# Kernel tuning notes

Hardware: AMD Instinct MI355X
Metric: run time of the kernel (lower is better)

Reference implementation:

```python
import jax, jax.numpy as jnp
import numpy as np

B, L, D_MODEL = 4, 4096, 1024
D_STATE, D_CONV, N_HEADS, CHUNK = 16, 4, 8, 64
D_INNER = 2048
HEADDIM = D_INNER // N_HEADS
CONV_DIM = D_INNER + 2 * D_STATE
D_PROJ = 2 * D_INNER + 2 * D_STATE + N_HEADS
EPS = 1e-5


def _silu(v):
    return v * jax.nn.sigmoid(v)


def _segsum(x):
    # x: (..., T) -> (..., T, T); segsum[i,j] = sum_{j<d<=i} x[d], -inf above diag
    T = x.shape[-1]
    xe = jnp.broadcast_to(x[..., None], (*x.shape, T))
    lower_strict = jnp.tril(jnp.ones((T, T), bool), -1)
    s = jnp.cumsum(jnp.where(lower_strict, xe, 0.0), axis=-2)
    lower = jnp.tril(jnp.ones((T, T), bool), 0)
    return jnp.where(lower, s, -jnp.inf)


def _ssd(x, A, Bm, Cm, chunk):
    # x: (b,l,h,p), A: (b,l,h), Bm/Cm: (b,l,n) (single B/C shared across heads)
    b, l, h, p = x.shape
    n = Bm.shape[-1]
    c = l // chunk
    x = x.reshape(b, c, chunk, h, p)
    A = A.reshape(b, c, chunk, h).transpose(0, 3, 1, 2)  # b h c l
    Bc = Bm.reshape(b, c, chunk, n)
    Cc = Cm.reshape(b, c, chunk, n)
    A_cs = jnp.cumsum(A, axis=-1)                        # b h c l
    Lmat = jnp.exp(_segsum(A))                           # b h c l s
    Y_diag = jnp.einsum('bcln,bcsn,bhcls,bcshp->bclhp', Cc, Bc, Lmat, x)
    decay_states = jnp.exp(A_cs[..., -1:] - A_cs)        # b h c l
    states = jnp.einsum('bcln,bhcl,bclhp->bchpn', Bc, decay_states, x)
    states = jnp.concatenate([jnp.zeros_like(states[:, :1]), states], axis=1)
    A_last = jnp.pad(A_cs[..., -1], ((0, 0), (0, 0), (1, 0)))  # b h (c+1)
    decay_chunk = jnp.exp(_segsum(A_last))               # b h (c+1) (c+1)
    new_states = jnp.einsum('bhzc,bchpn->bzhpn', decay_chunk, states)
    states_prev, final_state = new_states[:, :-1], new_states[:, -1]
    Y_off = jnp.einsum('bcln,bchpn,bhcl->bclhp', Cc, states_prev, jnp.exp(A_cs))
    Y = (Y_diag + Y_off).reshape(b, l, h, p)
    return Y, final_state


def setup_inputs() -> dict:
    key = jax.random.key(0)
    ks = jax.random.split(key, 8)
    inp = {
        'input_tensor': jax.random.normal(ks[0], (B, L, D_MODEL), dtype=jnp.float32),
        'W_in': jax.random.normal(ks[1], (D_PROJ, D_MODEL), dtype=jnp.float32) / np.sqrt(D_MODEL),
        'conv_w': jax.random.normal(ks[2], (CONV_DIM, 1, D_CONV), dtype=jnp.float32) * 0.2,
        'conv_b': jax.random.normal(ks[3], (CONV_DIM,), dtype=jnp.float32) * 0.02,
        'dt_bias': jax.random.uniform(ks[4], (N_HEADS,), dtype=jnp.float32) * 0.1,
        'log_A': jnp.log(jnp.arange(1, N_HEADS + 1, dtype=jnp.float32)),
        'D_skip': jnp.ones((N_HEADS,), dtype=jnp.float32),
        'norm_w': jnp.ones((D_INNER,), dtype=jnp.float32),
        'W_out': jax.random.normal(ks[5], (D_MODEL, D_INNER), dtype=jnp.float32) / np.sqrt(D_INNER),
    }
    return inp


def reference(input_tensor, W_in, conv_w, conv_b, dt_bias, log_A, D_skip, norm_w, W_out):
    bsz, slen, _ = input_tensor.shape
    proj = input_tensor @ W_in.T  # (b,l,D_PROJ)
    z = proj[..., :D_INNER]
    xBC = proj[..., D_INNER:D_INNER + CONV_DIM]
    dt = jax.nn.softplus(proj[..., D_INNER + CONV_DIM:] + dt_bias)  # (b,l,h)
    # causal depthwise conv1d (torch pads both sides then slices [:, :slen])
    xt = jnp.transpose(xBC, (0, 2, 1))  # (b,d,l)
    conv = jax.lax.conv_general_dilated(
        xt, conv_w, window_strides=(1,), padding=[(D_CONV - 1, 0)],
        feature_group_count=CONV_DIM) + conv_b[None, :, None]
    xBC = _silu(jnp.transpose(conv, (0, 2, 1)))
    x = xBC[..., :D_INNER]
    Bm = xBC[..., D_INNER:D_INNER + D_STATE]
    Cm = xBC[..., D_INNER + D_STATE:]
    A = jnp.broadcast_to((-jnp.exp(log_A))[None, None, :], (bsz, slen, N_HEADS))
    xh = x.reshape(bsz, slen, N_HEADS, HEADDIM) * dt[..., None]
    Y, _ = _ssd(xh, A, Bm, Cm, CHUNK)
    Y = Y + xh * D_skip[:, None]
    y = Y.reshape(bsz, slen, D_INNER)
    # gated RMSNorm
    y = y * _silu(z)
    y = y * jax.lax.rsqrt(jnp.mean(y * y, axis=-1, keepdims=True) + EPS) * norm_w
    return y @ W_out.T
```

## Files before the change

### kernel.cpp

```cpp
#include <hip/hip_runtime.h>
#include <hip/hip_bf16.h>
#include <math.h>

#define BATCH   4
#define SEQLEN  4096
#define DMODEL  1024
#define DSTATE  16
#define DCONV   4
#define NHEADS  8
#define CHUNKSZ 64
#define DINNER  2048
#define HEADDIM 256
#define CONVDIM 2080
#define DPROJ   4136
#define NPADW   4352
#define LDP     4224
#define ROWS    (BATCH*SEQLEN)
#define NCHUNK  (SEQLEN/CHUNKSZ)

typedef unsigned short bf16_t;
typedef __attribute__((ext_vector_type(8))) short bfrag;
typedef __attribute__((ext_vector_type(4))) float f32x4;

__device__ __forceinline__ float sigmoidf_(float v) { return 1.0f / (1.0f + __expf(-v)); }
__device__ __forceinline__ float siluf_(float v)    { return v * sigmoidf_(v); }
__device__ __forceinline__ float softplusf_(float v) {
    return fmaxf(v, 0.f) + log1pf(__expf(-fabsf(v)));
}

__device__ __forceinline__ float bf2f(bf16_t u) {
    union { unsigned int i; float f; } v; v.i = ((unsigned int)u) << 16; return v.f;
}
__device__ __forceinline__ float bflo(unsigned int u) {
    union { unsigned int i; float f; } v; v.i = u << 16; return v.f;
}
__device__ __forceinline__ float bfhi(unsigned int u) {
    union { unsigned int i; float f; } v; v.i = u & 0xffff0000u; return v.f;
}
__device__ __forceinline__ bf16_t f2bf(float f) {
    unsigned int x = __float_as_uint(f);
    unsigned int r = (x + 0x7fffu + ((x >> 16) & 1u)) >> 16;
    return (bf16_t)r;
}
__device__ __forceinline__ unsigned int pack2(float a, float b) {
    return (unsigned int)f2bf(a) | ((unsigned int)f2bf(b) << 16);
}

__device__ __forceinline__ void async_copy16(const bf16_t* g, bf16_t* l) {
    __builtin_amdgcn_global_load_lds(
        (const __attribute__((address_space(1))) void*)g,
        (__attribute__((address_space(3))) void*)l, 16, 0, 0);
}

template<int N>
__device__ __forceinline__ void wait_vmcnt() {
    __builtin_amdgcn_s_waitcnt(0x0F70 | N);
}
__device__ __forceinline__ void barrier_() {
    __builtin_amdgcn_s_barrier();
    asm volatile("" ::: "memory");
}

__global__ __launch_bounds__(256)
void cvt_f32_bf16(const float* __restrict__ src, bf16_t* __restrict__ dst, int n8)
{
    int i = blockIdx.x * 256 + threadIdx.x;
    if (i >= n8) return;
    float4 a = *(const float4*)&src[(size_t)i * 8];
    float4 b = *(const float4*)&src[(size_t)i * 8 + 4];
    uint4 o;
    o.x = pack2(a.x, a.y); o.y = pack2(a.z, a.w);
    o.z = pack2(b.x, b.y); o.w = pack2(b.z, b.w);
    *(uint4*)&dst[(size_t)i * 8] = o;
}

__global__ __launch_bounds__(256)
void cvt_pad_w1(const float* __restrict__ src, bf16_t* __restrict__ dst)
{
    int i = blockIdx.x * 256 + threadIdx.x;
    if (i >= NPADW * DMODEL / 4) return;
    size_t e = (size_t)i * 4;
    int row = (int)(e >> 10);
    ushort4 o = make_ushort4(0, 0, 0, 0);
    if (row < DPROJ) {
        float4 v = *(const float4*)&src[e];
        o.x = f2bf(v.x); o.y = f2bf(v.y); o.z = f2bf(v.z); o.w = f2bf(v.w);
    }
    *(ushort4*)&dst[e] = o;
}

__global__ __launch_bounds__(256)
void cvt_w2(const float* __restrict__ W, const float* __restrict__ norm_w,
            bf16_t* __restrict__ dst)
{
    int i = blockIdx.x * 256 + threadIdx.x;
    if (i >= DMODEL * DINNER / 4) return;
    size_t e = (size_t)i * 4;
    int k = (int)(e & (DINNER - 1));
    float4 v = *(const float4*)&W[e];
    float4 w = *(const float4*)&norm_w[k];
    ushort4 o;
    o.x = f2bf(v.x * w.x); o.y = f2bf(v.y * w.y);
    o.z = f2bf(v.z * w.z); o.w = f2bf(v.w * w.w);
    *(ushort4*)&dst[e] = o;
}

__device__ __forceinline__
void ld_afrags(bfrag (&af)[4][2], const bf16_t* base, int wmqi, int fr, int quad)
{
    #pragma unroll
    for (int i2 = 0; i2 < 4; ++i2)
        #pragma unroll
        for (int kk = 0; kk < 2; ++kk)
            af[i2][kk] = *(const bfrag*)
                &base[(wmqi + i2*16 + fr)*64 + (((kk*4 + quad) ^ (fr & 7)) * 8)];
}
__device__ __forceinline__
void ld_bfrags(bfrag (&bf_)[2][2], const bf16_t* base, int wnqj, int fr, int quad)
{
    #pragma unroll
    for (int j2 = 0; j2 < 2; ++j2)
        #pragma unroll
        for (int kk = 0; kk < 2; ++kk)
            bf_[j2][kk] = *(const bfrag*)
                &base[(wnqj + j2*16 + fr)*64 + (((kk*4 + quad) ^ (fr & 7)) * 8)];
}
template<int QI, int QJ>
__device__ __forceinline__
void mm8(f32x4 (&acc)[8][4], const bfrag (&af)[4][2], const bfrag (&bf_)[2][2])
{
    __builtin_amdgcn_s_setprio(1);
    #pragma unroll
    for (int i2 = 0; i2 < 4; ++i2)
        #pragma unroll
        for (int j2 = 0; j2 < 2; ++j2)
            #pragma unroll
            for (int kk = 0; kk < 2; ++kk)
                acc[QI*4 + i2][QJ*2 + j2] = __builtin_amdgcn_mfma_f32_16x16x32_bf16(
                    af[i2][kk], bf_[j2][kk], acc[QI*4 + i2][QJ*2 + j2], 0, 0, 0);
    __builtin_amdgcn_s_setprio(0);
}

template<bool OUT_BF16>
__device__ __forceinline__
void gemm256_body(const bf16_t* __restrict__ A, const bf16_t* __restrict__ W,
                  void* __restrict__ Cv, const float* __restrict__ rowScale,
                  int Nstore, int K, int lda, int ldw, int ldc)
{
    __shared__ __align__(16) bf16_t smem[65536];
    bf16_t* As = smem;
    bf16_t* Ws = smem + 32768;

    const int tid  = threadIdx.x;
    const int wave = tid >> 6, lane = tid & 63;
    const int quad = lane >> 4, fr = lane & 15;
    const int ln3  = lane >> 3;
    const int cswz = ((lane & 7) ^ ln3) * 8;

    const int gx   = gridDim.x;
    const int nwg  = gx * gridDim.y;
    const int flat = blockIdx.y * gx + blockIdx.x;
    const int q8   = nwg >> 3;
    const int swz  = (flat & 7) * q8 + (flat >> 3);
    const int col0 = (swz % gx) * 256;
    const int row0 = (swz / gx) * 256;

    const int wm = (wave >> 2) * 128, wn = (wave & 3) * 64;

    const bf16_t* gA[2][2];
    const bf16_t* gW[2][2];
    #pragma unroll
    for (int h = 0; h < 2; ++h)
        #pragma unroll
        for (int q = 0; q < 2; ++q) {
            int rA = 128*q + 8*wave + 64*h;
            int rB = 128*q + 64*(wave >> 2) + 8*(wave & 3) + 32*h;
            gA[h][q] = A + (size_t)(row0 + rA + ln3) * lda + cswz;
            gW[h][q] = W + (size_t)(col0 + rB + ln3) * ldw + cswz;
        }

#define STG_A(H, Q, NB, K0S)                                                     \
    async_copy16(gA[H][Q] + (K0S),                                               \
                 &As[(NB)*16384 + (128*(Q) + 8*wave + 64*(H))*64])
#define STG_B(H, Q, NB, K0S)                                                     \
    async_copy16(gW[H][Q] + (K0S),                                               \
                 &Ws[(NB)*16384 + (128*(Q) + 64*(wave>>2) + 8*(wave&3) + 32*(H))*64])

    f32x4 acc[8][4];
    #pragma unroll
    for (int i = 0; i < 8; ++i)
        #pragma unroll
        for (int j = 0; j < 4; ++j) {
            f32x4 z = {0.f, 0.f, 0.f, 0.f};
            acc[i][j] = z;
        }
    bfrag af[4][2], bf_[2][2];

    STG_A(0,0,0,0); STG_A(0,1,0,0);
    STG_B(0,0,0,0); STG_B(0,1,0,0);
    STG_B(1,0,0,0); STG_B(1,1,0,0);
    STG_A(1,0,0,0); STG_A(1,1,0,0);

#define TILE_STEP(BUF_, NB_, K0S_, STG_, V1_, V2_) do {                          \
          \
    wait_vmcnt<4>(); barrier_();                                                 \
    ld_afrags(af, &As[(BUF_)*16384], wm, fr, quad);                              \
    ld_bfrags(bf_, &Ws[(BUF_)*16384], wn, fr, quad);                             \
    if (STG_) { STG_A(0,0,NB_,K0S_); STG_A(0,1,NB_,K0S_); }                      \
    mm8<0,0>(acc, af, bf_);                                                      \
                                                     \
    wait_vmcnt<V1_>(); barrier_();                                               \
    ld_bfrags(bf_, &Ws[(BUF_)*16384], wn + 32, fr, quad);                        \
    if (STG_) { STG_B(0,0,NB_,K0S_); STG_B(0,1,NB_,K0S_); }                      \
    mm8<0,1>(acc, af, bf_);                                                      \
                                                     \
    wait_vmcnt<V2_>(); barrier_();                                               \
    ld_afrags(af, &As[(BUF_)*16384], wm + 64, fr, quad);                         \
    if (STG_) { STG_B(1,0,NB_,K0S_); STG_B(1,1,NB_,K0S_); }                      \
    mm8<1,1>(acc, af, bf_);                                                      \
                                     \
    barrier_();                                                                  \
    ld_bfrags(bf_, &Ws[(BUF_)*16384], wn, fr, quad);                             \
    if (STG_) { STG_A(1,0,NB_,K0S_); STG_A(1,1,NB_,K0S_); }                      \
    mm8<1,0>(acc, af, bf_);                                                      \
} while (0)

    const int nt = K >> 6;
    for (int t = 0; t < nt - 1; ++t) {
        TILE_STEP((t & 1), ((t & 1) ^ 1), ((t + 1) * 64), true, 4, 4);
    }
    TILE_STEP(((nt - 1) & 1), 0, 0, false, 2, 0);

#undef TILE_STEP
#undef STG_A
#undef STG_B

    if (OUT_BF16) {
        __syncthreads();
        bf16_t* C = (bf16_t*)Cv;
        #pragma unroll
        for (int pass = 0; pass < 2; ++pass) {
            if ((wave >> 2) == pass) {
                #pragma unroll
                for (int i = 0; i < 8; ++i)
                    #pragma unroll
                    for (int j = 0; j < 4; ++j) {
                        int col = wn + 16 * j + fr;
                        #pragma unroll
                        for (int r = 0; r < 4; ++r) {
                            int rl = 16 * i + quad * 4 + r;
                            smem[rl * 264 + col] = f2bf(acc[i][j][r]);
                        }
                    }
            }
            __syncthreads();
            #pragma unroll
            for (int k = 0; k < 8; ++k) {
                int id = k * 512 + tid;
                int rl = id >> 5, ch = id & 31;
                if (col0 + ch * 8 < Nstore) {
                    uint4 v = *(const uint4*)&smem[rl * 264 + ch * 8];
                    *(uint4*)&C[(size_t)(row0 + pass * 128 + rl) * ldc
                                + col0 + ch * 8] = v;
                }
            }
            if (pass == 0) __syncthreads();
        }
    } else {
        float rs[8][4];
        #pragma unroll
        for (int i = 0; i < 8; ++i) {
            size_t m = (size_t)row0 + wm + i * 16 + quad * 4;
            #pragma unroll
            for (int r = 0; r < 4; ++r) rs[i][r] = rowScale ? rowScale[m + r] : 1.f;
        }
        float* C = (float*)Cv;
        #pragma unroll
        for (int j = 0; j < 4; ++j) {
            int n = col0 + wn + j * 16 + fr;
            if (n < Nstore) {
                #pragma unroll
                for (int i = 0; i < 8; ++i) {
                    size_t m = (size_t)row0 + wm + i * 16 + quad * 4;
                    #pragma unroll
                    for (int r = 0; r < 4; ++r)
                        C[(m + r) * ldc + n] = acc[i][j][r] * rs[i][r];
                }
            }
        }
    }
}

__global__ __launch_bounds__(512, 2)
void gemm_g1(const bf16_t* __restrict__ A, const bf16_t* __restrict__ W,
             void* __restrict__ Cv, const float* __restrict__ rowScale,
             int Nstore, int K, int lda, int ldw, int ldc)
{ gemm256_body<true>(A, W, Cv, rowScale, Nstore, K, lda, ldw, ldc); }

__global__ __launch_bounds__(512, 2)
void gemm_g2(const bf16_t* __restrict__ A, const bf16_t* __restrict__ W,
             void* __restrict__ Cv, const float* __restrict__ rowScale,
             int Nstore, int K, int lda, int ldw, int ldc)
{ gemm256_body<false>(A, W, Cv, rowScale, Nstore, K, lda, ldw, ldc); }

__global__ __launch_bounds__(256)
void ssd_fused(const bf16_t* __restrict__ proj, const float* __restrict__ conv_w,
               const float* __restrict__ conv_b, const float* __restrict__ dt_bias,
               const float* __restrict__ log_A, const float* __restrict__ D_skip,
               bf16_t* __restrict__ ybuf)
{
    __shared__ float Bc[64][16];
    __shared__ float Cc[64][16];
    __shared__ float Bp[64][16];
    __shared__ float dtc[64];
    __shared__ float dtp[64];
    __shared__ __align__(16) bf16_t sc_b[64][72];
    __shared__ __align__(16) bf16_t xT[256][72];
    __shared__ __align__(16) bf16_t SpT[256][32];
    __shared__ __align__(16) bf16_t A2[64][32];

    const int c = blockIdx.x, h = blockIdx.y, b = blockIdx.z;
    const int t = threadIdx.x;
    const int row0 = b * SEQLEN + c * CHUNKSZ;
    const float a   = -__expf(log_A[h]);
    const float Dsk = D_skip[h];
    const float bias = dt_bias[h];

    {
        int s = t >> 2, ch8 = (t & 3) * 8;
        int l = c * CHUNKSZ + s;
        const bf16_t* base = &proj[(size_t)(row0 + s) * LDP + 4096 + ch8];
        uint4 zz = make_uint4(0, 0, 0, 0);
        uint4 u3 = *(const uint4*)&base[0];
        uint4 u2 = (l >= 1) ? *(const uint4*)&base[-LDP]     : zz;
        uint4 u1 = (l >= 2) ? *(const uint4*)&base[-2 * LDP] : zz;
        uint4 u0 = (l >= 3) ? *(const uint4*)&base[-3 * LDP] : zz;
        float t3[8] = {bflo(u3.x), bfhi(u3.x), bflo(u3.y), bfhi(u3.y),
                       bflo(u3.z), bfhi(u3.z), bflo(u3.w), bfhi(u3.w)};
        float t2[8] = {bflo(u2.x), bfhi(u2.x), bflo(u2.y), bfhi(u2.y),
                       bflo(u2.z), bfhi(u2.z), bflo(u2.w), bfhi(u2.w)};
        float t1[8] = {bflo(u1.x), bfhi(u1.x), bflo(u1.y), bfhi(u1.y),
                       bflo(u1.z), bfhi(u1.z), bflo(u1.w), bfhi(u1.w)};
        float t0[8] = {bflo(u0.x), bfhi(u0.x), bflo(u0.y), bfhi(u0.y),
                       bflo(u0.z), bfhi(u0.z), bflo(u0.w), bfhi(u0.w)};
        #pragma unroll
        for (int j = 0; j < 8; ++j) {
            int ch = ch8 + j;
            float4 w = *(const float4*)&conv_w[(2048 + ch) * 4];
            float av = conv_b[2048 + ch];
            av = fmaf(w.x, t0[j], av);
            av = fmaf(w.y, t1[j], av);
            av = fmaf(w.z, t2[j], av);
            av = fmaf(w.w, t3[j], av);
            float v = siluf_(av);
            if (ch < 16) Bc[s][ch] = v; else Cc[s][ch - 16] = v;
        }
    }
    if (t < 128) {
        int s = t >> 1, ch8 = (t & 1) * 8;
        float vout[8];
        #pragma unroll
        for (int j = 0; j < 8; ++j) vout[j] = 0.f;
        if (c > 0) {
            int l = (c - 1) * CHUNKSZ + s;
            const bf16_t* base = &proj[(size_t)(row0 - CHUNKSZ + s) * LDP + 4096 + ch8];
            uint4 zz = make_uint4(0, 0, 0, 0);
            uint4 u3 = *(const uint4*)&base[0];
            uint4 u2 = (l >= 1) ? *(const uint4*)&base[-LDP]     : zz;
            uint4 u1 = (l >= 2) ? *(const uint4*)&base[-2 * LDP] : zz;
            uint4 u0 = (l >= 3) ? *(const uint4*)&base[-3 * LDP] : zz;
            float t3[8] = {bflo(u3.x), bfhi(u3.x), bflo(u3.y), bfhi(u3.y),
                           bflo(u3.z), bfhi(u3.z), bflo(u3.w), bfhi(u3.w)};
            float t2[8] = {bflo(u2.x), bfhi(u2.x), bflo(u2.y), bfhi(u2.y),
                           bflo(u2.z), bfhi(u2.z), bflo(u2.w), bfhi(u2.w)};
            float t1[8] = {bflo(u1.x), bfhi(u1.x), bflo(u1.y), bfhi(u1.y),
                           bflo(u1.z), bfhi(u1.z), bflo(u1.w), bfhi(u1.w)};
            float t0[8] = {bflo(u0.x), bfhi(u0.x), bflo(u0.y), bfhi(u0.y),
                           bflo(u0.z), bfhi(u0.z), bflo(u0.w), bfhi(u0.w)};
            #pragma unroll
            for (int j = 0; j < 8; ++j) {
                int ch = ch8 + j;
                float4 w = *(const float4*)&conv_w[(2048 + ch) * 4];
                float av = conv_b[2048 + ch];
                av = fmaf(w.x, t0[j], av);
                av = fmaf(w.y, t1[j], av);
                av = fmaf(w.z, t2[j], av);
                av = fmaf(w.w, t3[j], av);
                vout[j] = siluf_(av);
            }
        }
        #pragma unroll
        for (int j = 0; j < 8; ++j) Bp[s][ch8 + j] = vout[j];
    } else if (t < 192) {
        int s = t - 128;
        float v = bf2f(proj[(size_t)(row0 + s) * LDP + 4128 + h]) + bias;
        dtc[s] = softplusf_(v);
    } else {
        int s = t - 192;
        float w = 0.f;
        if (c > 0) {
            float v = bf2f(proj[(size_t)(row0 - CHUNKSZ + s) * LDP + 4128 + h]) + bias;
            w = softplusf_(v) * __expf(a * (float)(63 - s));
        }
        dtp[s] = w;
    }
    __syncthreads();

    {
        int l = t >> 2;
        int sbase = (t & 3) * 16;
        unsigned int pk[8];
        #pragma unroll
        for (int jj = 0; jj < 16; jj += 2) {
            float v0 = 0.f, v1 = 0.f;
            int s0 = sbase + jj, s1 = s0 + 1;
            if (s0 <= l) {
                float dot = 0.f;
                #pragma unroll
                for (int n = 0; n < 16; ++n) dot = fmaf(Cc[l][n], Bc[s0][n], dot);
                v0 = dot * __expf(a * (float)(l - s0));
                if (s0 == l) v0 += Dsk;
            }
            if (s1 <= l) {
                float dot = 0.f;
                #pragma unroll
                for (int n = 0; n < 16; ++n) dot = fmaf(Cc[l][n], Bc[s1][n], dot);
                v1 = dot * __expf(a * (float)(l - s1));
                if (s1 == l) v1 += Dsk;
            }
            pk[jj >> 1] = pack2(v0, v1);
        }
        uint4 u0 = {pk[0], pk[1], pk[2], pk[3]};
        uint4 u1 = {pk[4], pk[5], pk[6], pk[7]};
        *(uint4*)&sc_b[l][sbase]     = u0;
        *(uint4*)&sc_b[l][sbase + 8] = u1;
    }
    if (t < 64) {
        float e = __expf(a * (float)(t + 1));
        unsigned int pk[8];
        #pragma unroll
        for (int n = 0; n < 16; n += 2) pk[n >> 1] = pack2(e * Cc[t][n], e * Cc[t][n + 1]);
        uint4 u0 = {pk[0], pk[1], pk[2], pk[3]};
        uint4 u1 = {pk[4], pk[5], pk[6], pk[7]};
        uint4 zz = make_uint4(0, 0, 0, 0);
        *(uint4*)&A2[t][0]  = u0;
        *(uint4*)&A2[t][8]  = u1;
        *(uint4*)&A2[t][16] = zz;
        *(uint4*)&A2[t][24] = zz;
    }

    {
        const int p = t;
        const int xch = h * HEADDIM + p;
        const float4 w = *(const float4*)&conv_w[(size_t)xch * 4];
        const float cb = conv_b[xch];
        const int colp = 2048 + xch;
        {
            const bf16_t* pr = &proj[(size_t)row0 * LDP + colp];
            int l0 = c * CHUNKSZ;
            float xm3 = (l0 >= 3) ? bf2f(pr[-3 * LDP]) : 0.f;
            float xm2 = (l0 >= 2) ? bf2f(pr[-2 * LDP]) : 0.f;
            float xm1 = (l0 >= 1) ? bf2f(pr[-LDP])     : 0.f;
            #pragma unroll
            for (int s0 = 0; s0 < 64; s0 += 8) {
                float xd[8];
                #pragma unroll
                for (int q = 0; q < 8; ++q) {
                    float xc = bf2f(pr[(size_t)(s0 + q) * LDP]);
                    float av = cb;
                    av = fmaf(w.x, xm3, av);
                    av = fmaf(w.y, xm2, av);
                    av = fmaf(w.z, xm1, av);
                    av = fmaf(w.w, xc, av);
                    xd[q] = siluf_(av) * dtc[s0 + q];
                    xm3 = xm2; xm2 = xm1; xm1 = xc;
                }
                uint4 u;
                u.x = pack2(xd[0], xd[1]); u.y = pack2(xd[2], xd[3]);
                u.z = pack2(xd[4], xd[5]); u.w = pack2(xd[6], xd[7]);
                *(uint4*)&xT[p][s0] = u;
            }
        }
        float Sp[16];
        #pragma unroll
        for (int n = 0; n < 16; ++n) Sp[n] = 0.f;
        if (c > 0) {
            const bf16_t* pr = &proj[(size_t)(row0 - CHUNKSZ) * LDP + colp];
            int l0 = (c - 1) * CHUNKSZ;
            float xm3 = (l0 >= 3) ? bf2f(pr[-3 * LDP]) : 0.f;
            float xm2 = (l0 >= 2) ? bf2f(pr[-2 * LDP]) : 0.f;
            float xm1 = (l0 >= 1) ? bf2f(pr[-LDP])     : 0.f;
            for (int s = 0; s < 64; ++s) {
                float xc = bf2f(pr[(size_t)s * LDP]);
                float av = cb;
                av = fmaf(w.x, xm3, av);
                av = fmaf(w.y, xm2, av);
                av = fmaf(w.z, xm1, av);
                av = fmaf(w.w, xc, av);
                float v = siluf_(av) * dtp[s];
                #pragma unroll
                for (int n = 0; n < 16; ++n) Sp[n] = fmaf(Bp[s][n], v, Sp[n]);
                xm3 = xm2; xm2 = xm1; xm1 = xc;
            }
        }
        unsigned int pk[8];
        #pragma unroll
        for (int n = 0; n < 16; n += 2) pk[n >> 1] = pack2(Sp[n], Sp[n + 1]);
        uint4 u0 = {pk[0], pk[1], pk[2], pk[3]};
        uint4 u1 = {pk[4], pk[5], pk[6], pk[7]};
        uint4 zz = make_uint4(0, 0, 0, 0);
        *(uint4*)&SpT[p][0]  = u0;
        *(uint4*)&SpT[p][8]  = u1;
        *(uint4*)&SpT[p][16] = zz;
        *(uint4*)&SpT[p][24] = zz;
    }
    __syncthreads();

    {
        const int wave = t >> 6, lane = t & 63;
        const int quad = lane >> 4, fr = lane & 15;
        f32x4 acc[4][4];
        #pragma unroll
        for (int i = 0; i < 4; ++i)
            #pragma unroll
            for (int j = 0; j < 4; ++j) {
                f32x4 z = {0.f, 0.f, 0.f, 0.f};
                acc[i][j] = z;
            }
        #pragma unroll
        for (int kk = 0; kk < 2; ++kk) {
            bfrag af[4], bfr[4];
            #pragma unroll
            for (int i = 0; i < 4; ++i)
                af[i] = *(const bfrag*)&sc_b[16 * i + fr][32 * kk + quad * 8];
            #pragma unroll
            for (int j = 0; j < 4; ++j)
                bfr[j] = *(const bfrag*)&xT[64 * wave + 16 * j + fr][32 * kk + quad * 8];
            #pragma unroll
            for (int i = 0; i < 4; ++i)
                #pragma unroll
                for (int j = 0; j < 4; ++j)
                    acc[i][j] = __builtin_amdgcn_mfma_f32_16x16x32_bf16(
                                    af[i], bfr[j], acc[i][j], 0, 0, 0);
        }
        {
            bfrag af[4], bfr[4];
            #pragma unroll
            for (int i = 0; i < 4; ++i)
                af[i] = *(const bfrag*)&A2[16 * i + fr][quad * 8];
            #pragma unroll
            for (int j = 0; j < 4; ++j)
                bfr[j] = *(const bfrag*)&SpT[64 * wave + 16 * j + fr][quad * 8];
            #pragma unroll
            for (int i = 0; i < 4; ++i)
                #pragma unroll
                for (int j = 0; j < 4; ++j)
                    acc[i][j] = __builtin_amdgcn_mfma_f32_16x16x32_bf16(
                                    af[i], bfr[j], acc[i][j], 0, 0, 0);
        }
        __syncthreads();
        bf16_t* buf = &xT[0][0];
        #pragma unroll
        for (int i = 0; i < 4; ++i)
            #pragma unroll
            for (int j = 0; j < 4; ++j) {
                int pc = 64 * wave + 16 * j + fr;
                #pragma unroll
                for (int r = 0; r < 4; ++r) {
                    int l = 16 * i + quad * 4 + r;
                    buf[l * 264 + pc] = f2bf(acc[i][j][r]);
                }
            }
        __syncthreads();
        bf16_t* ybase = &ybuf[(size_t)row0 * DINNER + h * HEADDIM];
        #pragma unroll
        for (int k = 0; k < 8; ++k) {
            int id = k * 256 + t;
            int l = id >> 5, ch = id & 31;
            uint4 v = *(const uint4*)&buf[l * 264 + ch * 8];
            *(uint4*)&ybase[(size_t)l * DINNER + ch * 8] = v;
        }
    }
}

__global__ __launch_bounds__(256)
void gate_kernel(const bf16_t* __restrict__ proj, bf16_t* __restrict__ ybuf,
                 float* __restrict__ rowscale)
{
    __shared__ float red[4];
    int i = blockIdx.x;
    int t = threadIdx.x;
    const bf16_t* zrow = &proj[(size_t)i * LDP];
    bf16_t* yrow = &ybuf[(size_t)i * DINNER];
    uint4 yv = *(const uint4*)&yrow[t * 8];
    uint4 zv = *(const uint4*)&zrow[t * 8];
    float ya[8] = {bflo(yv.x), bfhi(yv.x), bflo(yv.y), bfhi(yv.y),
                   bflo(yv.z), bfhi(yv.z), bflo(yv.w), bfhi(yv.w)};
    float za[8] = {bflo(zv.x), bfhi(zv.x), bflo(zv.y), bfhi(zv.y),
                   bflo(zv.z), bfhi(zv.z), bflo(zv.w), bfhi(zv.w)};
    float g[8];
    float ss = 0.f;
    #pragma unroll
    for (int j = 0; j < 8; ++j) {
        float gv = ya[j] * siluf_(za[j]);
        g[j] = gv;
        ss = fmaf(gv, gv, ss);
    }
    #pragma unroll
    for (int off = 32; off >= 1; off >>= 1) ss += __shfl_down(ss, off);
    if ((t & 63) == 0) red[t >> 6] = ss;
    __syncthreads();
    if (t == 0) {
        float tot = red[0] + red[1] + red[2] + red[3];
        rowscale[i] = rsqrtf(tot / (float)DINNER + 1e-5f);
    }
    uint4 o;
    o.x = pack2(g[0], g[1]); o.y = pack2(g[2], g[3]);
    o.z = pack2(g[4], g[5]); o.w = pack2(g[6], g[7]);
    *(uint4*)&yrow[t * 8] = o;
}

extern "C" void kernel_launch(void* const* d_in, const int* in_sizes, int n_in,
                              void* d_out, int out_size, void* d_ws, size_t ws_size,
                              hipStream_t stream)
{
    const float* input   = (const float*)d_in[0];
    const float* W_in    = (const float*)d_in[1];
    const float* conv_w  = (const float*)d_in[2];
    const float* conv_b  = (const float*)d_in[3];
    const float* dt_bias = (const float*)d_in[4];
    const float* log_A   = (const float*)d_in[5];
    const float* D_skip  = (const float*)d_in[6];
    const float* norm_w  = (const float*)d_in[7];
    const float* W_out   = (const float*)d_in[8];
    float* out = (float*)d_out;

    bf16_t* proj  = (bf16_t*)d_ws;
    bf16_t* region1 = proj + (size_t)ROWS * LDP;
    bf16_t* Wb2   = region1 + (size_t)ROWS * CONVDIM;
    float*  rowscale = (float*)(Wb2 + (size_t)DMODEL * DINNER);
    bf16_t* Ab    = region1;
    bf16_t* Wb1   = Ab + (size_t)ROWS * DMODEL;
    bf16_t* ybuf  = region1;

    size_t need = (size_t)ROWS * LDP * 2 + (size_t)ROWS * CONVDIM * 2
                + (size_t)DMODEL * DINNER * 2 + (size_t)ROWS * 4;
    if (ws_size < need) {
        hipMemsetAsync(d_out, 0, (size_t)out_size * sizeof(float), stream);
        return;
    }

    cvt_f32_bf16<<<(ROWS * DMODEL / 8 + 255) / 256, 256, 0, stream>>>(
        input, Ab, ROWS * DMODEL / 8);
    cvt_pad_w1<<<(NPADW * DMODEL / 4 + 255) / 256, 256, 0, stream>>>(W_in, Wb1);
    cvt_w2<<<(DMODEL * DINNER / 4 + 255) / 256, 256, 0, stream>>>(W_out, norm_w, Wb2);

    dim3 g1(NPADW / 256, ROWS / 256);
    gemm_g1<<<g1, 512, 0, stream>>>(Ab, Wb1, proj, nullptr,
                                    LDP, DMODEL, DMODEL, DMODEL, LDP);
    dim3 gs(NCHUNK, NHEADS, BATCH);
    ssd_fused<<<gs, 256, 0, stream>>>(proj, conv_w, conv_b, dt_bias,
                                      log_A, D_skip, ybuf);
    gate_kernel<<<ROWS, 256, 0, stream>>>(proj, ybuf, rowscale);
    dim3 g2(DMODEL / 256, ROWS / 256);
    gemm_g2<<<g2, 512, 0, stream>>>(ybuf, Wb2, out, rowscale,
                                    DMODEL, DINNER, DINNER, DINNER, DMODEL);
}
```

Measured before the change: 533.3 us.

## Switch GEMMs to 32x32 MFMA and fuse gating/RMS sum into SSD kernel

```diff
diff --git a/kernel.cpp b/kernel.cpp
--- a/kernel.cpp
+++ b/kernel.cpp
@@ -21,6 +21,7 @@
 typedef unsigned short bf16_t;
 typedef __attribute__((ext_vector_type(8))) short bfrag;
 typedef __attribute__((ext_vector_type(4))) float f32x4;
+typedef __attribute__((ext_vector_type(16))) float f32x16;
 
 __device__ __forceinline__ float sigmoidf_(float v) { return 1.0f / (1.0f + __expf(-v)); }
 __device__ __forceinline__ float siluf_(float v)    { return v * sigmoidf_(v); }
@@ -52,10 +53,7 @@
         (__attribute__((address_space(3))) void*)l, 16, 0, 0);
 }
 
-template<int N>
-__device__ __forceinline__ void wait_vmcnt() {
-    __builtin_amdgcn_s_waitcnt(0x0F70 | N);
-}
+#define WAITV(N)  asm volatile("s_waitcnt vmcnt(" #N ")" ::: "memory")
 __device__ __forceinline__ void barrier_() {
     __builtin_amdgcn_s_barrier();
     asm volatile("" ::: "memory");
@@ -106,45 +104,50 @@
 }
 
 __device__ __forceinline__
-void ld_afrags(bfrag (&af)[4][2], const bf16_t* base, int wmqi, int fr, int quad)
-{
+void ld_a32(bfrag (&a)[4][2], const bf16_t* base, int wm, int lane, int k0)
+{
+    const int r5 = lane & 31, hi = lane >> 5;
     #pragma unroll
-    for (int i2 = 0; i2 < 4; ++i2)
-        #pragma unroll
-        for (int kk = 0; kk < 2; ++kk)
-            af[i2][kk] = *(const bfrag*)
-                &base[(wmqi + i2*16 + fr)*64 + (((kk*4 + quad) ^ (fr & 7)) * 8)];
+    for (int ks = 0; ks < 2; ++ks)
+        #pragma unroll
+        for (int rb = 0; rb < 4; ++rb) {
+            int row = wm + rb * 32 + r5;
+            int chunk = (2 * (k0 + ks) + hi) ^ (row & 7);
+            a[rb][ks] = *(const bfrag*)&base[row * 64 + chunk * 8];
+        }
 }
 __device__ __forceinline__
-void ld_bfrags(bfrag (&bf_)[2][2], const bf16_t* base, int wnqj, int fr, int quad)
-{
+void ld_b32(bfrag (&b)[2][2], const bf16_t* base, int wn, int lane, int k0)
+{
+    const int r5 = lane & 31, hi = lane >> 5;
     #pragma unroll
-    for (int j2 = 0; j2 < 2; ++j2)
-        #pragma unroll
-        for (int kk = 0; kk < 2; ++kk)
-            bf_[j2][kk] = *(const bfrag*)
-                &base[(wnqj + j2*16 + fr)*64 + (((kk*4 + quad) ^ (fr & 7)) * 8)];
-}
-template<int QI, int QJ>
+    for (int ks = 0; ks < 2; ++ks)
+        #pragma unroll
+        for (int cb = 0; cb < 2; ++cb) {
+            int row = wn + cb * 32 + r5;
+            int chunk = (2 * (k0 + ks) + hi) ^ (row & 7);
+            b[cb][ks] = *(const bfrag*)&base[row * 64 + chunk * 8];
+        }
+}
 __device__ __forceinline__
-void mm8(f32x4 (&acc)[8][4], const bfrag (&af)[4][2], const bfrag (&bf_)[2][2])
+void mm16(f32x16 (&acc)[4][2], const bfrag (&a)[4][2], const bfrag (&b)[2][2])
 {
     __builtin_amdgcn_s_setprio(1);
     #pragma unroll
-    for (int i2 = 0; i2 < 4; ++i2)
-        #pragma unroll
-        for (int j2 = 0; j2 < 2; ++j2)
-            #pragma unroll
-            for (int kk = 0; kk < 2; ++kk)
-                acc[QI*4 + i2][QJ*2 + j2] = __builtin_amdgcn_mfma_f32_16x16x32_bf16(
-                    af[i2][kk], bf_[j2][kk], acc[QI*4 + i2][QJ*2 + j2], 0, 0, 0);
+    for (int ks = 0; ks < 2; ++ks)
+        #pragma unroll
+        for (int rb = 0; rb < 4; ++rb)
+            #pragma unroll
+            for (int cb = 0; cb < 2; ++cb)
+                acc[rb][cb] = __builtin_amdgcn_mfma_f32_32x32x16_bf16(
+                    a[rb][ks], b[cb][ks], acc[rb][cb], 0, 0, 0);
     __builtin_amdgcn_s_setprio(0);
 }
 
 template<bool OUT_BF16>
 __device__ __forceinline__
 void gemm256_body(const bf16_t* __restrict__ A, const bf16_t* __restrict__ W,
-                  void* __restrict__ Cv, const float* __restrict__ rowScale,
+                  void* __restrict__ Cv, const float* __restrict__ rowSum,
                   int Nstore, int K, int lda, int ldw, int ldc)
 {
     __shared__ __align__(16) bf16_t smem[65536];
@@ -153,7 +156,6 @@
 
     const int tid  = threadIdx.x;
     const int wave = tid >> 6, lane = tid & 63;
-    const int quad = lane >> 4, fr = lane & 15;
     const int ln3  = lane >> 3;
     const int cswz = ((lane & 7) ^ ln3) * 8;
 
@@ -186,55 +188,43 @@
     async_copy16(gW[H][Q] + (K0S),                                               \
                  &Ws[(NB)*16384 + (128*(Q) + 64*(wave>>2) + 8*(wave&3) + 32*(H))*64])
 
-    f32x4 acc[8][4];
+    f32x16 acc[4][2];
     #pragma unroll
-    for (int i = 0; i < 8; ++i)
-        #pragma unroll
-        for (int j = 0; j < 4; ++j) {
-            f32x4 z = {0.f, 0.f, 0.f, 0.f};
-            acc[i][j] = z;
-        }
-    bfrag af[4][2], bf_[2][2];
-
-    STG_A(0,0,0,0); STG_A(0,1,0,0);
-    STG_B(0,0,0,0); STG_B(0,1,0,0);
-    STG_B(1,0,0,0); STG_B(1,1,0,0);
-    STG_A(1,0,0,0); STG_A(1,1,0,0);
-
-#define TILE_STEP(BUF_, NB_, K0S_, STG_, V1_, V2_) do {                          \
-          \
-    wait_vmcnt<4>(); barrier_();                                                 \
-    ld_afrags(af, &As[(BUF_)*16384], wm, fr, quad);                              \
-    ld_bfrags(bf_, &Ws[(BUF_)*16384], wn, fr, quad);                             \
-    if (STG_) { STG_A(0,0,NB_,K0S_); STG_A(0,1,NB_,K0S_); }                      \
-    mm8<0,0>(acc, af, bf_);                                                      \
-                                                     \
-    wait_vmcnt<V1_>(); barrier_();                                               \
-    ld_bfrags(bf_, &Ws[(BUF_)*16384], wn + 32, fr, quad);                        \
-    if (STG_) { STG_B(0,0,NB_,K0S_); STG_B(0,1,NB_,K0S_); }                      \
-    mm8<0,1>(acc, af, bf_);                                                      \
-                                                     \
-    wait_vmcnt<V2_>(); barrier_();                                               \
-    ld_afrags(af, &As[(BUF_)*16384], wm + 64, fr, quad);                         \
-    if (STG_) { STG_B(1,0,NB_,K0S_); STG_B(1,1,NB_,K0S_); }                      \
-    mm8<1,1>(acc, af, bf_);                                                      \
-                                     \
-    barrier_();                                                                  \
-    ld_bfrags(bf_, &Ws[(BUF_)*16384], wn, fr, quad);                             \
-    if (STG_) { STG_A(1,0,NB_,K0S_); STG_A(1,1,NB_,K0S_); }                      \
-    mm8<1,0>(acc, af, bf_);                                                      \
-} while (0)
+    for (int i = 0; i < 4; ++i)
+        #pragma unroll
+        for (int j = 0; j < 2; ++j)
+            #pragma unroll
+            for (int r = 0; r < 16; ++r)
+                acc[i][j][r] = 0.f;
+    bfrag afr[4][2], bfr[2][2];
+
+    STG_A(0,0,0,0); STG_A(0,1,0,0); STG_A(1,0,0,0); STG_A(1,1,0,0);
+    STG_B(0,0,0,0); STG_B(0,1,0,0); STG_B(1,0,0,0); STG_B(1,1,0,0);
 
     const int nt = K >> 6;
-    for (int t = 0; t < nt - 1; ++t) {
-        TILE_STEP((t & 1), ((t & 1) ^ 1), ((t + 1) * 64), true, 4, 4);
-    }
-    TILE_STEP(((nt - 1) & 1), 0, 0, false, 2, 0);
-
-#undef TILE_STEP
+    for (int t = 0; t < nt; ++t) {
+        const int cur = (t & 1) * 16384;
+        const int nb  = (t + 1) & 1;
+        const int ko  = (t + 1) * 64;
+        const bool stg = (t + 1 < nt);
+        WAITV(0);
+        barrier_();
+        ld_a32(afr, As + cur, wm, lane, 0);
+        ld_b32(bfr, Ws + cur, wn, lane, 0);
+        if (stg) { STG_A(0,0,nb,ko); STG_A(0,1,nb,ko);
+                   STG_A(1,0,nb,ko); STG_A(1,1,nb,ko); }
+        mm16(acc, afr, bfr);
+        ld_a32(afr, As + cur, wm, lane, 2);
+        ld_b32(bfr, Ws + cur, wn, lane, 2);
+        if (stg) { STG_B(0,0,nb,ko); STG_B(0,1,nb,ko);
+                   STG_B(1,0,nb,ko); STG_B(1,1,nb,ko); }
+        mm16(acc, afr, bfr);
+    }
+
 #undef STG_A
 #undef STG_B
 
+    const int c32 = lane & 31, hi4 = (lane >> 5) * 4;
     if (OUT_BF16) {
         __syncthreads();
         bf16_t* C = (bf16_t*)Cv;
@@ -242,14 +232,14 @@
         for (int pass = 0; pass < 2; ++pass) {
             if ((wave >> 2) == pass) {
                 #pragma unroll
-                for (int i = 0; i < 8; ++i)
+                for (int rb = 0; rb < 4; ++rb)
                     #pragma unroll
-                    for (int j = 0; j < 4; ++j) {
-                        int col = wn + 16 * j + fr;
+                    for (int cb = 0; cb < 2; ++cb) {
+                        int col = wn + cb * 32 + c32;
                         #pragma unroll
-                        for (int r = 0; r < 4; ++r) {
-                            int rl = 16 * i + quad * 4 + r;
-                            smem[rl * 264 + col] = f2bf(acc[i][j][r]);
+                        for (int reg = 0; reg < 16; ++reg) {
+                            int rl = rb * 32 + (reg & 3) + 8 * (reg >> 2) + hi4;
+                            smem[rl * 264 + col] = f2bf(acc[rb][cb][reg]);
                         }
                     }
             }
@@ -267,24 +257,26 @@
             if (pass == 0) __syncthreads();
         }
     } else {
-        float rs[8][4];
-        #pragma unroll
-        for (int i = 0; i < 8; ++i) {
-            size_t m = (size_t)row0 + wm + i * 16 + quad * 4;
-            #pragma unroll
-            for (int r = 0; r < 4; ++r) rs[i][r] = rowScale ? rowScale[m + r] : 1.f;
-        }
         float* C = (float*)Cv;
         #pragma unroll
-        for (int j = 0; j < 4; ++j) {
-            int n = col0 + wn + j * 16 + fr;
-            if (n < Nstore) {
-                #pragma unroll
-                for (int i = 0; i < 8; ++i) {
-                    size_t m = (size_t)row0 + wm + i * 16 + quad * 4;
+        for (int rb = 0; rb < 4; ++rb) {
+            float rs[16];
+            #pragma unroll
+            for (int reg = 0; reg < 16; ++reg) {
+                size_t m = (size_t)row0 + wm + rb * 32
+                         + (reg & 3) + 8 * (reg >> 2) + hi4;
+                rs[reg] = rowSum ? rsqrtf(rowSum[m] * (1.f / DINNER) + 1e-5f) : 1.f;
+            }
+            #pragma unroll
+            for (int cb = 0; cb < 2; ++cb) {
+                int n = col0 + wn + cb * 32 + c32;
+                if (n < Nstore) {
                     #pragma unroll
-                    for (int r = 0; r < 4; ++r)
-                        C[(m + r) * ldc + n] = acc[i][j][r] * rs[i][r];
+                    for (int reg = 0; reg < 16; ++reg) {
+                        size_t m = (size_t)row0 + wm + rb * 32
+                                 + (reg & 3) + 8 * (reg >> 2) + hi4;
+                        C[m * ldc + n] = acc[rb][cb][reg] * rs[reg];
+                    }
                 }
             }
         }
@@ -293,21 +285,21 @@
 
 __global__ __launch_bounds__(512, 2)
 void gemm_g1(const bf16_t* __restrict__ A, const bf16_t* __restrict__ W,
-             void* __restrict__ Cv, const float* __restrict__ rowScale,
+             void* __restrict__ Cv, const float* __restrict__ rowSum,
              int Nstore, int K, int lda, int ldw, int ldc)
-{ gemm256_body<true>(A, W, Cv, rowScale, Nstore, K, lda, ldw, ldc); }
+{ gemm256_body<true>(A, W, Cv, rowSum, Nstore, K, lda, ldw, ldc); }
 
 __global__ __launch_bounds__(512, 2)
 void gemm_g2(const bf16_t* __restrict__ A, const bf16_t* __restrict__ W,
-             void* __restrict__ Cv, const float* __restrict__ rowScale,
+             void* __restrict__ Cv, const float* __restrict__ rowSum,
              int Nstore, int K, int lda, int ldw, int ldc)
-{ gemm256_body<false>(A, W, Cv, rowScale, Nstore, K, lda, ldw, ldc); }
+{ gemm256_body<false>(A, W, Cv, rowSum, Nstore, K, lda, ldw, ldc); }
 
 __global__ __launch_bounds__(256)
 void ssd_fused(const bf16_t* __restrict__ proj, const float* __restrict__ conv_w,
                const float* __restrict__ conv_b, const float* __restrict__ dt_bias,
                const float* __restrict__ log_A, const float* __restrict__ D_skip,
-               bf16_t* __restrict__ ybuf)
+               bf16_t* __restrict__ ybuf, float* __restrict__ rowsum)
 {
     __shared__ float Bc[64][16];
     __shared__ float Cc[64][16];
@@ -573,51 +565,34 @@
             }
         __syncthreads();
         bf16_t* ybase = &ybuf[(size_t)row0 * DINNER + h * HEADDIM];
+        const bf16_t* zbase = &proj[(size_t)row0 * LDP + h * HEADDIM];
         #pragma unroll
         for (int k = 0; k < 8; ++k) {
             int id = k * 256 + t;
             int l = id >> 5, ch = id & 31;
-            uint4 v = *(const uint4*)&buf[l * 264 + ch * 8];
-            *(uint4*)&ybase[(size_t)l * DINNER + ch * 8] = v;
-        }
-    }
-}
-
-__global__ __launch_bounds__(256)
-void gate_kernel(const bf16_t* __restrict__ proj, bf16_t* __restrict__ ybuf,
-                 float* __restrict__ rowscale)
-{
-    __shared__ float red[4];
-    int i = blockIdx.x;
-    int t = threadIdx.x;
-    const bf16_t* zrow = &proj[(size_t)i * LDP];
-    bf16_t* yrow = &ybuf[(size_t)i * DINNER];
-    uint4 yv = *(const uint4*)&yrow[t * 8];
-    uint4 zv = *(const uint4*)&zrow[t * 8];
-    float ya[8] = {bflo(yv.x), bfhi(yv.x), bflo(yv.y), bfhi(yv.y),
-                   bflo(yv.z), bfhi(yv.z), bflo(yv.w), bfhi(yv.w)};
-    float za[8] = {bflo(zv.x), bfhi(zv.x), bflo(zv.y), bfhi(zv.y),
-                   bflo(zv.z), bfhi(zv.z), bflo(zv.w), bfhi(zv.w)};
-    float g[8];
-    float ss = 0.f;
-    #pragma unroll
-    for (int j = 0; j < 8; ++j) {
-        float gv = ya[j] * siluf_(za[j]);
-        g[j] = gv;
-        ss = fmaf(gv, gv, ss);
-    }
-    #pragma unroll
-    for (int off = 32; off >= 1; off >>= 1) ss += __shfl_down(ss, off);
-    if ((t & 63) == 0) red[t >> 6] = ss;
-    __syncthreads();
-    if (t == 0) {
-        float tot = red[0] + red[1] + red[2] + red[3];
-        rowscale[i] = rsqrtf(tot / (float)DINNER + 1e-5f);
-    }
-    uint4 o;
-    o.x = pack2(g[0], g[1]); o.y = pack2(g[2], g[3]);
-    o.z = pack2(g[4], g[5]); o.w = pack2(g[6], g[7]);
-    *(uint4*)&yrow[t * 8] = o;
+            uint4 yv = *(const uint4*)&buf[l * 264 + ch * 8];
+            uint4 zv = *(const uint4*)&zbase[(size_t)l * LDP + ch * 8];
+            float ya[8] = {bflo(yv.x), bfhi(yv.x), bflo(yv.y), bfhi(yv.y),
+                           bflo(yv.z), bfhi(yv.z), bflo(yv.w), bfhi(yv.w)};
+            float za[8] = {bflo(zv.x), bfhi(zv.x), bflo(zv.y), bfhi(zv.y),
+                           bflo(zv.z), bfhi(zv.z), bflo(zv.w), bfhi(zv.w)};
+            float g[8];
+            float ss = 0.f;
+            #pragma unroll
+            for (int j = 0; j < 8; ++j) {
+                float gv = ya[j] * siluf_(za[j]);
+                g[j] = gv;
+                ss = fmaf(gv, gv, ss);
+            }
+            uint4 o;
+            o.x = pack2(g[0], g[1]); o.y = pack2(g[2], g[3]);
+            o.z = pack2(g[4], g[5]); o.w = pack2(g[6], g[7]);
+            *(uint4*)&ybase[(size_t)l * DINNER + ch * 8] = o;
+            #pragma unroll
+            for (int off = 16; off >= 1; off >>= 1) ss += __shfl_xor(ss, off, 32);
+            if ((t & 31) == 0) atomicAdd(&rowsum[row0 + l], ss);
+        }
+    }
 }
 
 extern "C" void kernel_launch(void* const* d_in, const int* in_sizes, int n_in,
@@ -638,7 +613,7 @@
     bf16_t* proj  = (bf16_t*)d_ws;
     bf16_t* region1 = proj + (size_t)ROWS * LDP;
     bf16_t* Wb2   = region1 + (size_t)ROWS * CONVDIM;
-    float*  rowscale = (float*)(Wb2 + (size_t)DMODEL * DINNER);
+    float*  rowsum = (float*)(Wb2 + (size_t)DMODEL * DINNER);
     bf16_t* Ab    = region1;
     bf16_t* Wb1   = Ab + (size_t)ROWS * DMODEL;
     bf16_t* ybuf  = region1;
@@ -654,15 +629,15 @@
         input, Ab, ROWS * DMODEL / 8);
     cvt_pad_w1<<<(NPADW * DMODEL / 4 + 255) / 256, 256, 0, stream>>>(W_in, Wb1);
     cvt_w2<<<(DMODEL * DINNER / 4 + 255) / 256, 256, 0, stream>>>(W_out, norm_w, Wb2);
+    hipMemsetAsync(rowsum, 0, (size_t)ROWS * sizeof(float), stream);
 
     dim3 g1(NPADW / 256, ROWS / 256);
     gemm_g1<<<g1, 512, 0, stream>>>(Ab, Wb1, proj, nullptr,
                                     LDP, DMODEL, DMODEL, DMODEL, LDP);
     dim3 gs(NCHUNK, NHEADS, BATCH);
     ssd_fused<<<gs, 256, 0, stream>>>(proj, conv_w, conv_b, dt_bias,
-                                      log_A, D_skip, ybuf);
-    gate_kernel<<<ROWS, 256, 0, stream>>>(proj, ybuf, rowscale);
+                                      log_A, D_skip, ybuf, rowsum);
     dim3 g2(DMODEL / 256, ROWS / 256);
-    gemm_g2<<<g2, 512, 0, stream>>>(ybuf, Wb2, out, rowscale,
+    gemm_g2<<<g2, 512, 0, stream>>>(ybuf, Wb2, out, rowsum,
                                     DMODEL, DINNER, DINNER, DINNER, DMODEL);
 }
```

Measured after the change: 541.4 us. Within noise of the previous version (+1.5%).
